# Optimization experiments

Hardware: AMD Instinct MI355X
Metric: run time of the kernel (lower is better)

The kernel has to match this reference:

```python
import jax, jax.numpy as jnp
import numpy as np

SEQ, BATCH = 512, 128
FEAT_CH, EMBED = 1024, 1024
N_LANG = 8  # tgt_lang_toks = [0..7]


def setup_inputs() -> dict:
    key = jax.random.key(0)
    k_feat, k_tok, k_w, k_b = jax.random.split(key, 4)
    feat = jax.random.normal(k_feat, (SEQ, BATCH, FEAT_CH), dtype=jnp.float32)
    tgt_lang_toks = jax.random.randint(k_tok, (BATCH,), 0, N_LANG, dtype=jnp.int64)
    # stacked per-language Linear params: W[l] is [embed, feat] (torch Linear layout), b[l] is [embed]
    bound = 1.0 / np.sqrt(FEAT_CH)
    W = jax.random.uniform(k_w, (N_LANG, EMBED, FEAT_CH), minval=-bound, maxval=bound, dtype=jnp.float32)
    b = jax.random.uniform(k_b, (N_LANG, EMBED), minval=-bound, maxval=bound, dtype=jnp.float32)
    return {"feat": feat, "W": W, "b": b, "tgt_lang_toks": tgt_lang_toks}


def reference(feat, W, b, tgt_lang_toks):
    # Each batch column uses the Linear of its language token. Since the
    # language token values equal their index in tgt_lang_toks=[0..7], the
    # per-group mask/gather/scatter of the original collapses to a per-batch
    # weight gather + batched matmul (grouped GEMM as dense dispatch).
    toks = tgt_lang_toks.astype(jnp.int32)
    W_sel = W[toks]          # [B, E, F]
    b_sel = b[toks]          # [B, E]
    # [S,B,F] x [B,E,F] -> [S,B,E]
    out = jnp.einsum('sbf,bef->sbe', feat, W_sel) + b_sel[None, :, :]
    return out
```

## Files before the change

kernel.cpp:

```cpp
#include <hip/hip_runtime.h>
#include <hip/hip_bf16.h>

#define SEQ   512
#define BATCH 128
#define FEAT  1024
#define EMBED 1024
#define NLANG 8

typedef __attribute__((ext_vector_type(8))) short bf16x8;
typedef __attribute__((ext_vector_type(4))) float f32x4;
typedef unsigned short ushort_t;

__device__ __forceinline__ unsigned pk2(float a, float b) {
  float2 f; f.x = a; f.y = b;
  __hip_bfloat162 h = __float22bfloat162_rn(f);
  union { __hip_bfloat162 h2; unsigned u; } cv;
  cv.h2 = h;
  return cv.u;
}

__device__ __forceinline__ bf16x8 cvt8(float4 lo, float4 hi) {
  union { bf16x8 v; unsigned u[4]; } q;
  q.u[0] = pk2(lo.x, lo.y); q.u[1] = pk2(lo.z, lo.w);
  q.u[2] = pk2(hi.x, hi.y); q.u[3] = pk2(hi.z, hi.w);
  return q.v;
}

__device__ __forceinline__ void gld16(const void* g, void* l) {
  __builtin_amdgcn_global_load_lds(
      (const __attribute__((address_space(1))) void*)g,
      (__attribute__((address_space(3))) void*)l, 16, 0, 0);
}

__global__ __launch_bounds__(256) void convert_w_kernel(
    const float* __restrict__ Wf, ushort_t* __restrict__ Wbf)
{
  const int n = (NLANG * EMBED * FEAT) / 4;
  for (int c = blockIdx.x * 256 + threadIdx.x; c < n; c += gridDim.x * 256) {
    float4 v = ((const float4*)Wf)[c];
    uint2 o; o.x = pk2(v.x, v.y); o.y = pk2(v.z, v.w);
    *(uint2*)(Wbf + ((size_t)c << 2)) = o;
  }
}

__global__ __launch_bounds__(512, 4) void grouped_gemm_fused(
    const float* __restrict__ feat,
    const ushort_t* __restrict__ Wbf,
    const float* __restrict__ bias,
    const int*   __restrict__ toks,
    float*       __restrict__ out)
{
  extern __shared__ char ldsraw[];
  ushort_t* Alds = (ushort_t*)ldsraw;
  ushort_t* Blds = (ushort_t*)(ldsraw + 24576);
  __shared__ int tokarr[128];
  __shared__ unsigned long long ballots[2][8];
  __shared__ int perm[128];
  __shared__ int rowsrc[128];

  const int tid = threadIdx.x;
  const int l   = tid & 63;
  const int w   = tid >> 6;
  const int wr  = w >> 2;
  const int wc  = w & 3;

  const int bid = blockIdx.x;
  const int L   = (bid & 7) * 256 + (bid >> 3);
  const int et  = L & 3;
  const int mt  = L >> 2;
  const int m0  = mt * 128;
  const int e0  = et * 256;

  if (tid < 128) tokarr[tid] = toks[tid];
  __syncthreads();
  if (tid < 128) {
    int myt = tokarr[tid];
#pragma unroll
    for (int lg = 0; lg < 8; ++lg) {
      unsigned long long bl = __ballot(myt == lg);
      if (l == 0) ballots[w][lg] = bl;
    }
  }
  __syncthreads();

  int lsel = 0, base = 0, csel = 1, boff_sel = 0;
  {
    int cum = 0, boff = 0;
#pragma unroll
    for (int lg = 0; lg < 8; ++lg) {
      int c = __popcll(ballots[0][lg]) + __popcll(ballots[1][lg]);
      int seg = c << 9;
      bool in = (m0 >= cum) && (m0 < cum + seg);
      if (in) { lsel = lg; base = cum; csel = c; boff_sel = boff; }
      cum += seg; boff += c;
    }
  }

  if (tid < 128) {
    int myt = tokarr[tid];
    unsigned long long ltm = (1ull << l) - 1ull;
    int rank = (w == 0) ? __popcll(ballots[0][myt] & ltm)
                        : __popcll(ballots[0][myt]) + __popcll(ballots[1][myt] & ltm);
    int boff2 = 0;
#pragma unroll
    for (int lg = 0; lg < 8; ++lg) {
      int c = __popcll(ballots[0][lg]) + __popcll(ballots[1][lg]);
      boff2 += (lg < myt) ? c : 0;
    }
    perm[boff2 + rank] = tid;
  }
  __syncthreads();
  if (tid < 128) {
    int local = m0 - base + tid;
    int s = local / csel;
    int j = local - s * csel;
    rowsrc[tid] = s * BATCH + perm[boff_sel + j];
  }
  __syncthreads();

  const int arow = tid >> 2;
  const int aq   = tid & 2 ? (tid & 3) : (tid & 3);
  const float* aSrcP = feat + (size_t)rowsrc[arow] * FEAT + (tid & 3) * 8;
  const int wchunk = arow * 4 + ((tid & 3) ^ ((arow >> 1) & 3));
  float4 ar0, ar1;
  (void)aq;

  const int ch  = w * 128 + l;
  const int rwB = ch >> 2;
  const int ccB = ch & 3;
  const int sB  = (rwB >> 1) & 3;
  const ushort_t* bS0 = Wbf + ((size_t)lsel * EMBED + e0 + rwB) * FEAT + ((ccB ^ sB) * 8);
  const ushort_t* bS1 = bS0 + (size_t)16 * FEAT;
  const int bD0 = (w * 128) * 8;
  const int bD1 = (w * 128 + 64) * 8;

  const int kc  = l >> 4;
  const int rA  = wr * 64 + (l & 15);
  const int aRd = rA * 32 + ((kc ^ ((rA >> 1) & 3)) * 8);
  const int rB  = wc * 64 + (l & 15);
  const int bRd = rB * 32 + ((kc ^ ((rB >> 1) & 3)) * 8);

  f32x4 acc[4][4] = {};

#define LOAD_A(kt)                                                         \
  do { const float* _p = aSrcP + (kt) * 32;                                \
    ar0 = *(const float4*)(_p); ar1 = *(const float4*)(_p + 4); } while (0)
#define WRITE_A(buf)                                                       \
  do { ((bf16x8*)(Alds + (buf) * 4096))[wchunk] = cvt8(ar0, ar1); } while (0)
#define STAGE_B(kt, buf)                                                   \
  do { const int _o = (kt) * 32;                                           \
    gld16(bS0 + _o, Blds + (buf) * 8192 + bD0);                            \
    gld16(bS1 + _o, Blds + (buf) * 8192 + bD1); } while (0)

#define BODY(t, J, DOWRITE, DOLOAD, ENDWAIT, ENDBAR)                       \
  do {                                                                     \
    if (DOWRITE) { WRITE_A(((J) + 1) % 3); }                               \
    if (DOLOAD)  { LOAD_A((t) + 2); STAGE_B((t) + 2, ((J) + 2) % 3); }     \
    const ushort_t* Ar_ = Alds + (J) * 4096;                               \
    const ushort_t* Br_ = Blds + (J) * 8192;                               \
    bf16x8 af[4], bfq[4];                                                  \
    _Pragma("unroll") for (int mf = 0; mf < 4; ++mf)                       \
        af[mf] = *(const bf16x8*)(Ar_ + aRd + mf * 512);                   \
    _Pragma("unroll") for (int nf = 0; nf < 4; ++nf)                       \
        bfq[nf] = *(const bf16x8*)(Br_ + bRd + nf * 512);                  \
    __builtin_amdgcn_s_setprio(1);                                         \
    _Pragma("unroll") for (int mf = 0; mf < 4; ++mf)                       \
        _Pragma("unroll") for (int nf = 0; nf < 4; ++nf)                   \
            acc[mf][nf] = __builtin_amdgcn_mfma_f32_16x16x32_bf16(         \
                af[mf], bfq[nf], acc[mf][nf], 0, 0, 0);                    \
    __builtin_amdgcn_s_setprio(0);                                         \
    asm volatile(ENDWAIT ::: "memory");                                    \
    if (ENDBAR) { __builtin_amdgcn_s_barrier();                            \
                  __builtin_amdgcn_sched_barrier(0); }                     \
  } while (0)

  LOAD_A(0);
  WRITE_A(0);
  STAGE_B(0, 0);
  STAGE_B(1, 1);
  LOAD_A(1);
  asm volatile("s_waitcnt vmcnt(4) lgkmcnt(0)" ::: "memory");
  __builtin_amdgcn_s_barrier();
  __builtin_amdgcn_sched_barrier(0);

#pragma unroll 1
  for (int gg = 0; gg < 10; ++gg) {
    const int g = gg * 3;
    BODY(g + 0, 0, true, true, "s_waitcnt vmcnt(4) lgkmcnt(0)", true);
    BODY(g + 1, 1, true, true, "s_waitcnt vmcnt(4) lgkmcnt(0)", true);
    BODY(g + 2, 2, true, true, "s_waitcnt vmcnt(4) lgkmcnt(0)", true);
  }
  BODY(30, 0, true, false, "s_waitcnt vmcnt(0) lgkmcnt(0)", true);
  BODY(31, 1, false, false, "s_nop 0", false);

#undef BODY
#undef LOAD_A
#undef WRITE_A
#undef STAGE_B

  const int col = l & 15;
  const int r4  = (l >> 4) * 4;
  float bvv[4];
#pragma unroll
  for (int nf = 0; nf < 4; ++nf)
    bvv[nf] = bias[lsel * EMBED + e0 + wc * 64 + nf * 16 + col];
#pragma unroll
  for (int mf = 0; mf < 4; ++mf) {
#pragma unroll
    for (int j = 0; j < 4; ++j) {
      const size_t ro = (size_t)rowsrc[wr * 64 + mf * 16 + r4 + j] * EMBED;
#pragma unroll
      for (int nf = 0; nf < 4; ++nf)
        out[ro + e0 + wc * 64 + nf * 16 + col] = acc[mf][nf][j] + bvv[nf];
    }
  }
}

__global__ __launch_bounds__(256, 2) void grouped_proj_fused(
    const float* __restrict__ feat, const float* __restrict__ Wt,
    const float* __restrict__ bias, const int* __restrict__ toks,
    float* __restrict__ out)
{
  __shared__ uint4 As[1024];
  __shared__ uint4 Bs[1024];
  __shared__ int tokarr[128];
  __shared__ unsigned long long ballots[2][8];
  __shared__ int perm[128];
  __shared__ int rowsrc[128];

  const int tid  = threadIdx.x;
  const int lane = tid & 63;
  const int wv   = tid >> 6;
  const int wr   = wv >> 1;
  const int wc   = wv & 1;
  const int bid = blockIdx.x;
  const int xcd = bid & 7;
  const int sq  = bid >> 3;
  const int et  = sq & 7;
  const int mt  = (sq >> 3) * 8 + xcd;
  const int m0  = mt * 128;
  const int e0  = et * 128;

  if (tid < 128) tokarr[tid] = toks[tid];
  __syncthreads();
  if (tid < 128) {
    int myt = tokarr[tid];
#pragma unroll
    for (int lg = 0; lg < 8; ++lg) {
      unsigned long long bl = __ballot(myt == lg);
      if (lane == 0) ballots[wv][lg] = bl;
    }
  }
  __syncthreads();
  int lsel = 0, base = 0, csel = 1, boff_sel = 0;
  {
    int cum = 0, boff = 0;
#pragma unroll
    for (int lg = 0; lg < 8; ++lg) {
      int c = __popcll(ballots[0][lg]) + __popcll(ballots[1][lg]);
      int seg = c << 9;
      bool in = (m0 >= cum) && (m0 < cum + seg);
      if (in) { lsel = lg; base = cum; csel = c; boff_sel = boff; }
      cum += seg; boff += c;
    }
  }
  if (tid < 128) {
    int myt = tokarr[tid];
    unsigned long long ltm = (1ull << lane) - 1ull;
    int rank = (wv == 0) ? __popcll(ballots[0][myt] & ltm)
                         : __popcll(ballots[0][myt]) + __popcll(ballots[1][myt] & ltm);
    int boff2 = 0;
#pragma unroll
    for (int lg = 0; lg < 8; ++lg) {
      int c = __popcll(ballots[0][lg]) + __popcll(ballots[1][lg]);
      boff2 += (lg < myt) ? c : 0;
    }
    perm[boff2 + rank] = tid;
  }
  __syncthreads();
  if (tid < 128) {
    int local = m0 - base + tid;
    int s = local / csel;
    int j = local - s * csel;
    rowsrc[tid] = s * BATCH + perm[boff_sel + j];
  }
  __syncthreads();

  int slot_i[4];
  const float* aptr[4];
  const float* bptr[4];
#pragma unroll
  for (int it = 0; it < 4; ++it) {
    int c    = it * 256 + tid;
    int kg   = c & 7;
    int row  = c >> 3;
    int ksub = kg & 3;
    int kk   = kg >> 2;
    int frag = row >> 4;
    slot_i[it] = (kk * 8 + frag) * 64 + ((row & 15) ^ (ksub << 1) ^ kk) + ksub * 16;
    aptr[it] = feat + (size_t)rowsrc[row] * FEAT + kg * 8;
    bptr[it] = Wt + ((size_t)lsel * EMBED + e0 + row) * FEAT + kg * 8;
  }

  f32x4 acc[4][4] = {};
  for (int k0 = 0; k0 < FEAT; k0 += 64) {
    __syncthreads();
#pragma unroll
    for (int it = 0; it < 4; ++it) {
      float4 alo = *(const float4*)(aptr[it] + k0);
      float4 ahi = *(const float4*)(aptr[it] + k0 + 4);
      uint4 av;
      av.x = pk2(alo.x, alo.y); av.y = pk2(alo.z, alo.w);
      av.z = pk2(ahi.x, ahi.y); av.w = pk2(ahi.z, ahi.w);
      As[slot_i[it]] = av;
      float4 blo = *(const float4*)(bptr[it] + k0);
      float4 bhi = *(const float4*)(bptr[it] + k0 + 4);
      uint4 bv;
      bv.x = pk2(blo.x, blo.y); bv.y = pk2(blo.z, blo.w);
      bv.z = pk2(bhi.x, bhi.y); bv.w = pk2(bhi.z, bhi.w);
      Bs[slot_i[it]] = bv;
    }
    __syncthreads();
#pragma unroll
    for (int kk = 0; kk < 2; ++kk) {
      const int ksr = lane >> 4;
      const int sw  = ((lane & 15) ^ (ksr << 1) ^ kk) + ksr * 16;
      bf16x8 af[4], bfr[4];
#pragma unroll
      for (int mi = 0; mi < 4; ++mi)
        af[mi] = ((const bf16x8*)As)[(kk * 8 + wr * 4 + mi) * 64 + sw];
#pragma unroll
      for (int ni = 0; ni < 4; ++ni)
        bfr[ni] = ((const bf16x8*)Bs)[(kk * 8 + wc * 4 + ni) * 64 + sw];
#pragma unroll
      for (int mi = 0; mi < 4; ++mi)
#pragma unroll
        for (int ni = 0; ni < 4; ++ni)
          acc[mi][ni] = __builtin_amdgcn_mfma_f32_16x16x32_bf16(
              af[mi], bfr[ni], acc[mi][ni], 0, 0, 0);
    }
  }

  const int col = lane & 15;
  const int r0  = (lane >> 4) * 4;
  float bvv[4];
#pragma unroll
  for (int ni = 0; ni < 4; ++ni)
    bvv[ni] = bias[lsel * EMBED + e0 + wc * 64 + ni * 16 + col];
#pragma unroll
  for (int mi = 0; mi < 4; ++mi) {
#pragma unroll
    for (int j = 0; j < 4; ++j) {
      const size_t ro = (size_t)rowsrc[wr * 64 + mi * 16 + r0 + j] * EMBED;
#pragma unroll
      for (int ni = 0; ni < 4; ++ni)
        out[ro + e0 + wc * 64 + ni * 16 + col] = acc[mi][ni][j] + bvv[ni];
    }
  }
}

extern "C" void kernel_launch(void* const* d_in, const int* in_sizes, int n_in,
                              void* d_out, int out_size, void* d_ws, size_t ws_size,
                              hipStream_t stream) {
  const float* feat = (const float*)d_in[0];
  const float* W    = (const float*)d_in[1];
  const float* bias = (const float*)d_in[2];
  const int*   toks = (const int*)d_in[3];
  float* out = (float*)d_out;

  const size_t wbf_bytes = (size_t)NLANG * EMBED * FEAT * 2;

  if (ws_size >= wbf_bytes) {
    ushort_t* Wbf = (ushort_t*)d_ws;
    convert_w_kernel<<<512, 256, 0, stream>>>(W, Wbf);
    (void)hipFuncSetAttribute((const void*)grouped_gemm_fused,
                              hipFuncAttributeMaxDynamicSharedMemorySize, 73728);
    const int nblk = (SEQ * BATCH / 128) * (EMBED / 256);
    grouped_gemm_fused<<<nblk, 512, 73728, stream>>>(feat, Wbf, bias, toks, out);
  } else {
    grouped_proj_fused<<<(SEQ * BATCH / 128) * (EMBED / 128), 256, 0, stream>>>(
        feat, W, bias, toks, out);
  }
}
```

Measured before the change: 257.3 us.

## Enlarge GEMM block tile to 256x256 with 16 waves per block

Doubles the block's M tile from 128 to 256 rows and raises the block to 1024 threads (16 waves), halving the grid. It reworks LDS into a double-buffered A tile and a triple-buffered B tile, with the A swizzle moved to the global-load side. This lets each staged B tile be reused across twice as many rows, cutting weight traffic per output. In exchange it uses more LDS per block, which may lower occupancy, and the memory wait counts change.

```diff
diff --git a/kernel.cpp b/kernel.cpp
--- a/kernel.cpp
+++ b/kernel.cpp
@@ -43,20 +43,18 @@
   }
 }
 
-__global__ __launch_bounds__(512, 4) void grouped_gemm_fused(
+__global__ __launch_bounds__(1024, 4) void grouped_gemm_fused16(
     const float* __restrict__ feat,
     const ushort_t* __restrict__ Wbf,
     const float* __restrict__ bias,
     const int*   __restrict__ toks,
     float*       __restrict__ out)
 {
-  extern __shared__ char ldsraw[];
-  ushort_t* Alds = (ushort_t*)ldsraw;
-  ushort_t* Blds = (ushort_t*)(ldsraw + 24576);
+  extern __shared__ ushort_t lds[];
   __shared__ int tokarr[128];
   __shared__ unsigned long long ballots[2][8];
   __shared__ int perm[128];
-  __shared__ int rowsrc[128];
+  __shared__ int rowsrc[256];
 
   const int tid = threadIdx.x;
   const int l   = tid & 63;
@@ -65,10 +63,10 @@
   const int wc  = w & 3;
 
   const int bid = blockIdx.x;
-  const int L   = (bid & 7) * 256 + (bid >> 3);
+  const int L   = (bid & 7) * 128 + (bid >> 3);
   const int et  = L & 3;
-  const int mt  = L >> 2;
-  const int m0  = mt * 128;
+  const int mt  = (L >> 7) * 32 + ((L >> 2) & 31);
+  const int m0  = mt * 256;
   const int e0  = et * 256;
 
   if (tid < 128) tokarr[tid] = toks[tid];
@@ -110,7 +108,7 @@
     perm[boff2 + rank] = tid;
   }
   __syncthreads();
-  if (tid < 128) {
+  if (tid < 256) {
     int local = m0 - base + tid;
     int s = local / csel;
     int j = local - s * csel;
@@ -119,20 +117,17 @@
   __syncthreads();
 
   const int arow = tid >> 2;
-  const int aq   = tid & 2 ? (tid & 3) : (tid & 3);
-  const float* aSrcP = feat + (size_t)rowsrc[arow] * FEAT + (tid & 3) * 8;
-  const int wchunk = arow * 4 + ((tid & 3) ^ ((arow >> 1) & 3));
+  const int acck = tid & 3;
+  const int sAk  = (arow >> 1) & 3;
+  const float* aSrcP = feat + (size_t)rowsrc[arow] * FEAT + ((acck ^ sAk) * 8);
+  const int wchunk = tid;
   float4 ar0, ar1;
-  (void)aq;
-
-  const int ch  = w * 128 + l;
-  const int rwB = ch >> 2;
-  const int ccB = ch & 3;
-  const int sB  = (rwB >> 1) & 3;
-  const ushort_t* bS0 = Wbf + ((size_t)lsel * EMBED + e0 + rwB) * FEAT + ((ccB ^ sB) * 8);
-  const ushort_t* bS1 = bS0 + (size_t)16 * FEAT;
-  const int bD0 = (w * 128) * 8;
-  const int bD1 = (w * 128 + 64) * 8;
+
+  const int rwB = tid >> 2;
+  const int ccB = tid & 3;
+  const int sBk = (rwB >> 1) & 3;
+  const ushort_t* bS = Wbf + ((size_t)lsel * EMBED + e0 + rwB) * FEAT + ((ccB ^ sBk) * 8);
+  const int dOffB = w * 512;
 
   const int kc  = l >> 4;
   const int rA  = wr * 64 + (l & 15);
@@ -145,19 +140,17 @@
 #define LOAD_A(kt)                                                         \
   do { const float* _p = aSrcP + (kt) * 32;                                \
     ar0 = *(const float4*)(_p); ar1 = *(const float4*)(_p + 4); } while (0)
-#define WRITE_A(buf)                                                       \
-  do { ((bf16x8*)(Alds + (buf) * 4096))[wchunk] = cvt8(ar0, ar1); } while (0)
-#define STAGE_B(kt, buf)                                                   \
-  do { const int _o = (kt) * 32;                                           \
-    gld16(bS0 + _o, Blds + (buf) * 8192 + bD0);                            \
-    gld16(bS1 + _o, Blds + (buf) * 8192 + bD1); } while (0)
-
-#define BODY(t, J, DOWRITE, DOLOAD, ENDWAIT, ENDBAR)                       \
+#define WRITE_A(abuf)                                                      \
+  do { ((bf16x8*)(lds + (abuf) * 8192))[wchunk] = cvt8(ar0, ar1); } while (0)
+#define STAGE_B(kt, bbuf)                                                  \
+  do { gld16(bS + (kt) * 32, lds + 16384 + (bbuf) * 8192 + dOffB); } while (0)
+
+#define BODY(t, AJ, BJ, DOWRITE, DOLOAD, ENDWAIT, ENDBAR)                  \
   do {                                                                     \
-    if (DOWRITE) { WRITE_A(((J) + 1) % 3); }                               \
-    if (DOLOAD)  { LOAD_A((t) + 2); STAGE_B((t) + 2, ((J) + 2) % 3); }     \
-    const ushort_t* Ar_ = Alds + (J) * 4096;                               \
-    const ushort_t* Br_ = Blds + (J) * 8192;                               \
+    if (DOWRITE) { WRITE_A((AJ) ^ 1); }                                    \
+    if (DOLOAD)  { LOAD_A((t) + 2); STAGE_B((t) + 2, ((BJ) + 2) % 3); }    \
+    const ushort_t* Ar_ = lds + (AJ) * 8192;                               \
+    const ushort_t* Br_ = lds + 16384 + (BJ) * 8192;                       \
     bf16x8 af[4], bfq[4];                                                  \
     _Pragma("unroll") for (int mf = 0; mf < 4; ++mf)                       \
         af[mf] = *(const bf16x8*)(Ar_ + aRd + mf * 512);                   \
@@ -176,22 +169,24 @@
 
   LOAD_A(0);
   WRITE_A(0);
+  LOAD_A(1);
   STAGE_B(0, 0);
   STAGE_B(1, 1);
-  LOAD_A(1);
-  asm volatile("s_waitcnt vmcnt(4) lgkmcnt(0)" ::: "memory");
+  asm volatile("s_waitcnt vmcnt(1) lgkmcnt(0)" ::: "memory");
   __builtin_amdgcn_s_barrier();
   __builtin_amdgcn_sched_barrier(0);
 
 #pragma unroll 1
-  for (int gg = 0; gg < 10; ++gg) {
-    const int g = gg * 3;
-    BODY(g + 0, 0, true, true, "s_waitcnt vmcnt(4) lgkmcnt(0)", true);
-    BODY(g + 1, 1, true, true, "s_waitcnt vmcnt(4) lgkmcnt(0)", true);
-    BODY(g + 2, 2, true, true, "s_waitcnt vmcnt(4) lgkmcnt(0)", true);
-  }
-  BODY(30, 0, true, false, "s_waitcnt vmcnt(0) lgkmcnt(0)", true);
-  BODY(31, 1, false, false, "s_nop 0", false);
+  for (int gb = 0; gb < 30; gb += 6) {
+    BODY(gb + 0, 0, 0, true, true, "s_waitcnt vmcnt(3) lgkmcnt(0)", true);
+    BODY(gb + 1, 1, 1, true, true, "s_waitcnt vmcnt(3) lgkmcnt(0)", true);
+    BODY(gb + 2, 0, 2, true, true, "s_waitcnt vmcnt(3) lgkmcnt(0)", true);
+    BODY(gb + 3, 1, 0, true, true, "s_waitcnt vmcnt(3) lgkmcnt(0)", true);
+    BODY(gb + 4, 0, 1, true, true, "s_waitcnt vmcnt(3) lgkmcnt(0)", true);
+    BODY(gb + 5, 1, 2, true, true, "s_waitcnt vmcnt(3) lgkmcnt(0)", true);
+  }
+  BODY(30, 0, 0, true, false, "s_waitcnt vmcnt(0) lgkmcnt(0)", true);
+  BODY(31, 1, 1, false, false, "s_nop 0", false);
 
 #undef BODY
 #undef LOAD_A
@@ -373,10 +368,10 @@
   if (ws_size >= wbf_bytes) {
     ushort_t* Wbf = (ushort_t*)d_ws;
     convert_w_kernel<<<512, 256, 0, stream>>>(W, Wbf);
-    (void)hipFuncSetAttribute((const void*)grouped_gemm_fused,
-                              hipFuncAttributeMaxDynamicSharedMemorySize, 73728);
-    const int nblk = (SEQ * BATCH / 128) * (EMBED / 256);
-    grouped_gemm_fused<<<nblk, 512, 73728, stream>>>(feat, Wbf, bias, toks, out);
+    (void)hipFuncSetAttribute((const void*)grouped_gemm_fused16,
+                              hipFuncAttributeMaxDynamicSharedMemorySize, 81920);
+    const int nblk = (SEQ * BATCH / 256) * (EMBED / 256);
+    grouped_gemm_fused16<<<nblk, 1024, 81920, stream>>>(feat, Wbf, bias, toks, out);
   } else {
     grouped_proj_fused<<<(SEQ * BATCH / 128) * (EMBED / 128), 256, 0, stream>>>(
         feat, W, bias, toks, out);
```

After: 297.4 us. 1.16x slower.
